# Kernel tuning notes

Measured on AMD Instinct MI355X. Metric: run time of the kernel, lower is better.

Reference implementation:

```python
import jax, jax.numpy as jnp
import numpy as np

B, S, D, H, HD, K, FF, G, E = 2, 2048, 512, 8, 64, 31, 2048, 4, 2
EPS = 1e-6


def _layer_norm(x, scale, bias):
    m = jnp.mean(x, axis=-1, keepdims=True)
    v = jnp.var(x, axis=-1, keepdims=True)
    return (x - m) * jax.lax.rsqrt(v + EPS) * scale + bias


def _forward(x, group_ids, p):
    (ln1_s, ln1_b, ck, cb, ln2_s, ln2_b,
     wq, bq, wk, bk, wv, bv, wo, bo, w1, b1, w2, b2) = p
    # ---- conv sublayer: LN -> Conv1d(SAME) -> gelu -> residual ----
    r = x
    h = _layer_norm(x, ln1_s, ln1_b)
    h = jax.lax.conv_general_dilated(h, ck, (1,), 'SAME',
                                     dimension_numbers=('NWC', 'WIO', 'NWC')) + cb
    x = jax.nn.gelu(h) + r
    # ---- self-attention sublayer: LN -> MHA -> residual ----
    r = x
    h = _layer_norm(x, ln2_s, ln2_b)
    q = jnp.einsum('bsd,dhk->bshk', h, wq) + bq   # [B,S,H,HD]
    k = jnp.einsum('bsd,dhk->bshk', h, wk) + bk
    v = jnp.einsum('bsd,dhk->bshk', h, wv) + bv
    scale = jnp.asarray(1.0 / np.sqrt(HD), h.dtype)
    att = jax.nn.softmax(jnp.einsum('bqhk,bshk->bhqs', q, k) * scale, axis=-1)
    o = jnp.einsum('bhqs,bshk->bqhk', att, v)
    x = jnp.einsum('bqhk,hkd->bqd', o, wo) + bo + r
    # ---- MoE sublayer: group tokens -> per-group experts -> mean -> combine ----
    r = x
    xf = x.reshape(-1, D)            # [N, D]
    gid = group_ids.reshape(-1)      # [N]
    # Each token routed by group_id gets the mean over that group's E experts.
    hid = jax.nn.gelu(jnp.einsum('nd,gedf->genf', xf, w1) + b1[:, :, None, :])  # [G,E,N,FF]
    ye = jnp.einsum('genf,gefd->gend', hid, w2) + b2[:, :, None, :]             # [G,E,N,D]
    yg = ye.mean(axis=1)                                                        # [G,N,D]
    sel = yg[gid, jnp.arange(gid.shape[0])]                                     # [N,D] combine by group id
    return sel.reshape(B, S, D) + r


def setup_inputs() -> dict:
    key = jax.random.key(0)
    ks = jax.random.split(key, 12)
    std = 0.02
    f32 = jnp.float32
    return {
        'x': jax.random.normal(ks[0], (B, S, D), f32),
        'group_ids': jax.random.randint(ks[1], (B, S), 0, G, jnp.int32),
        'ln1_scale': jnp.ones((D,), f32), 'ln1_bias': jnp.zeros((D,), f32),
        'conv_kernel': jax.random.normal(ks[2], (K, D, D), f32) * std,
        'conv_bias': jnp.zeros((D,), f32),
        'ln2_scale': jnp.ones((D,), f32), 'ln2_bias': jnp.zeros((D,), f32),
        'wq': jax.random.normal(ks[3], (D, H, HD), f32) * std, 'bq': jnp.zeros((H, HD), f32),
        'wk': jax.random.normal(ks[4], (D, H, HD), f32) * std, 'bk': jnp.zeros((H, HD), f32),
        'wv': jax.random.normal(ks[5], (D, H, HD), f32) * std, 'bv': jnp.zeros((H, HD), f32),
        'wo': jax.random.normal(ks[6], (H, HD, D), f32) * std, 'bo': jnp.zeros((D,), f32),
        'w1': jax.random.normal(ks[7], (G, E, D, FF), f32) * std, 'b1': jnp.zeros((G, E, FF), f32),
        'w2': jax.random.normal(ks[8], (G, E, FF, D), f32) * std, 'b2': jnp.zeros((G, E, D), f32),
    }


def reference(x, group_ids, ln1_scale, ln1_bias, conv_kernel, conv_bias,
              ln2_scale, ln2_bias, wq, bq, wk, bk, wv, bv, wo, bo,
              w1, b1, w2, b2):
    p = (ln1_scale, ln1_bias, conv_kernel, conv_bias, ln2_scale, ln2_bias,
         wq, bq, wk, bk, wv, bv, wo, bo, w1, b1, w2, b2)
    return _forward(x, group_ids, p)
```

## Files before the change

kernel.cpp:

```cpp
#include <hip/hip_runtime.h>
#include <hip/hip_bf16.h>
#include <math.h>
#include <stdint.h>

namespace {

constexpr int B_ = 2, S_ = 2048, D_ = 512, H_ = 8, HD_ = 64, K_ = 31,
              FF_ = 2048, G_ = 4, E_ = 2;
constexpr int N_ = B_ * S_;
constexpr int SP_ = S_ + 30;
constexpr float EPS_ = 1e-6f;
constexpr int PADCAP_ = 4608;

typedef __bf16 bf16x8 __attribute__((ext_vector_type(8)));
typedef unsigned short u16x8 __attribute__((ext_vector_type(8)));
typedef unsigned short u16x4 __attribute__((ext_vector_type(4)));
typedef float f32x4 __attribute__((ext_vector_type(4)));

__device__ __forceinline__ uint16_t f2bf(float f) {
  union { float f; uint32_t u; } v; v.f = f;
  uint32_t r = v.u + 0x7FFFu + ((v.u >> 16) & 1u);
  return (uint16_t)(r >> 16);
}
__device__ __forceinline__ float bf2f(uint16_t u) {
  union { uint32_t u; float f; } v; v.u = (uint32_t)u << 16;
  return v.f;
}

__device__ __forceinline__ float gelu_f(float x) {
  const float c = 0.7978845608028654f;
  return 0.5f * x * (1.0f + tanhf(c * (x + 0.044715f * x * x * x)));
}

#define GLOAD_LDS16(gsrc, ldst)                                              \
  __builtin_amdgcn_global_load_lds(                                          \
      (const __attribute__((address_space(1))) void*)(gsrc),                 \
      (__attribute__((address_space(3))) void*)(ldst), 16, 0, 0)

#define VMCNT(n) asm volatile("s_waitcnt vmcnt(" #n ")" ::: "memory")
#define MEMBAR asm volatile("" ::: "memory")
#define BARRIER __builtin_amdgcn_s_barrier()

__device__ __forceinline__ void kstep_swz(const char* As, const char* Bs,
                                          int wr, int wc, int l15, int g,
                                          f32x4 acc[4][4]) {
#pragma unroll
  for (int ks = 0; ks < 2; ++ks) {
    int co = (((ks << 2) | g) ^ (l15 & 7)) << 4;
    bf16x8 a[4], b[4];
#pragma unroll
    for (int m = 0; m < 4; ++m)
      a[m] = *(const bf16x8*)(As + (wr * 64 + m * 16 + l15) * 128 + co);
#pragma unroll
    for (int n = 0; n < 4; ++n)
      b[n] = *(const bf16x8*)(Bs + (wc * 64 + n * 16 + l15) * 128 + co);
#pragma unroll
    for (int m = 0; m < 4; ++m)
#pragma unroll
      for (int n = 0; n < 4; ++n)
        acc[m][n] = __builtin_amdgcn_mfma_f32_16x16x32_bf16(a[m], b[n], acc[m][n], 0, 0, 0);
  }
}

template <int NK>
__device__ __forceinline__ void gemm_k_dbuf64(const uint16_t* Ab, int lda,
                                              const uint16_t* Bb, int ldb,
                                              int t, int wr, int wc, int l15, int g,
                                              uint16_t (*As)[8192], uint16_t (*Bs)[8192],
                                              f32x4 acc[4][4]) {
  int r8 = t >> 3, clog = (t & 7) ^ (r8 & 7);
  int ubase = (t & ~63) * 8;
  auto stage = [&](int k0, int buf) {
#pragma unroll
    for (int pi = 0; pi < 4; ++pi) {
      int row = pi * 32 + r8;
      GLOAD_LDS16(Ab + (size_t)row * lda + k0 + clog * 8, As[buf] + pi * 2048 + ubase);
      GLOAD_LDS16(Bb + (size_t)row * ldb + k0 + clog * 8, Bs[buf] + pi * 2048 + ubase);
    }
  };
  stage(0, 0);
  int cur = 0;
  for (int ki = 0; ki < NK; ++ki) {
    if (ki + 1 < NK) {
      stage((ki + 1) * 64, cur ^ 1);
      VMCNT(8);
    } else {
      VMCNT(0);
    }
    BARRIER; MEMBAR;
    kstep_swz((const char*)As[cur], (const char*)Bs[cur], wr, wc, l15, g, acc);
    MEMBAR; BARRIER;
    cur ^= 1;
  }
}

__global__ __launch_bounds__(256) void prep_kernel(
    const float* __restrict__ ck, const float* __restrict__ wq,
    const float* __restrict__ wk, const float* __restrict__ wv,
    const float* __restrict__ wo, const float* __restrict__ w1,
    const float* __restrict__ w2, uint16_t* __restrict__ ckT,
    uint16_t* __restrict__ wqkvT, uint16_t* __restrict__ woT,
    uint16_t* __restrict__ w1T, uint16_t* __restrict__ w2T,
    uint16_t* __restrict__ Hpad, uint16_t* __restrict__ x2bf) {
  int bi = blockIdx.x, t = threadIdx.x;
  if (bi >= 25344) {
    int j4 = bi - 25344;
    uint16_t* dst;
    if (j4 < 60) {
      int b = j4 / 30, j = j4 % 30;
      int row = b * SP_ + (j < 15 ? j : 2048 + j);
      dst = Hpad + (size_t)row * D_;
    } else {
      dst = x2bf + (size_t)N_ * D_;
    }
    dst[t] = 0;
    dst[t + 256] = 0;
    return;
  }
  const float* src;
  uint16_t* dst;
  int R, C, r0, c0;
  if (bi < 7936) {
    int z = bi >> 8, tile = bi & 255;
    R = 512; C = 512;
    c0 = (tile & 15) * 32; r0 = (tile >> 4) * 32;
    src = ck + (size_t)z * 262144; dst = ckT + (size_t)z * 262144;
  } else if (bi < 8960) {
    int idx = bi - 7936, mat = idx >> 8, tile = idx & 255;
    R = 512; C = 512;
    c0 = (tile & 15) * 32; r0 = (tile >> 4) * 32;
    src = mat == 0 ? wq : (mat == 1 ? wk : (mat == 2 ? wv : wo));
    dst = mat == 3 ? woT : wqkvT + (size_t)mat * 262144;
  } else if (bi < 17152) {
    int idx = bi - 8960, z = idx >> 10, tile = idx & 1023;
    R = 512; C = 2048;
    c0 = (tile & 63) * 32; r0 = (tile >> 6) * 32;
    src = w1 + (size_t)z * 1048576; dst = w1T + (size_t)z * 1048576;
  } else {
    int idx = bi - 17152, z = idx >> 10, tile = idx & 1023;
    R = 2048; C = 512;
    c0 = (tile & 15) * 32; r0 = (tile >> 4) * 32;
    src = w2 + (size_t)z * 1048576; dst = w2T + (size_t)z * 1048576;
  }
  __shared__ float tile[32][33];
  int tc = t & 31, tr = t >> 5;
#pragma unroll
  for (int i = 0; i < 4; ++i) {
    int r = tr + i * 8;
    tile[r][tc] = src[(size_t)(r0 + r) * C + c0 + tc];
  }
  __syncthreads();
#pragma unroll
  for (int i = 0; i < 4; ++i) {
    int rr = tr + i * 8;
    dst[(size_t)(c0 + rr) * R + r0 + tc] = f2bf(tile[tc][rr]);
  }
}

__global__ __launch_bounds__(256) void ln_bf16_kernel(
    const float* __restrict__ in, uint16_t* __restrict__ out,
    const float* __restrict__ scale, const float* __restrict__ bias, int hpad) {
  int row = blockIdx.x;
  const float* xr = in + (size_t)row * D_;
  int t = threadIdx.x;
  float v0 = xr[t], v1 = xr[t + 256];
  float s = v0 + v1, sq = v0 * v0 + v1 * v1;
  for (int o = 32; o > 0; o >>= 1) {
    s += __shfl_down(s, o);
    sq += __shfl_down(sq, o);
  }
  __shared__ float sm[8];
  __shared__ float mr[2];
  int lane = t & 63, wid = t >> 6;
  if (lane == 0) { sm[wid] = s; sm[wid + 4] = sq; }
  __syncthreads();
  if (t == 0) {
    float ts = sm[0] + sm[1] + sm[2] + sm[3];
    float tq = sm[4] + sm[5] + sm[6] + sm[7];
    float m = ts / D_;
    mr[0] = m;
    mr[1] = rsqrtf(tq / D_ - m * m + EPS_);
  }
  __syncthreads();
  float m = mr[0], rs = mr[1];
  size_t drow = hpad ? ((size_t)(row >> 11) * SP_ + 15 + (row & 2047)) : (size_t)row;
  uint16_t* orow = out + drow * D_;
  orow[t] = f2bf((v0 - m) * rs * scale[t] + bias[t]);
  orow[t + 256] = f2bf((v1 - m) * rs * scale[t + 256] + bias[t + 256]);
}

__global__ __launch_bounds__(512) void conv_mfma_kernel(
    const uint16_t* __restrict__ Hpad, const uint16_t* __restrict__ ckT,
    uint16_t* __restrict__ Pout) {
  __shared__ __align__(16) uint16_t As[2][20480];
  __shared__ __align__(16) uint16_t Bs[2][16384];
  int bid = blockIdx.x;
  int ks = bid & 7, tmn = bid >> 3, tm = tmn & 15, tn = tmn >> 4;
  int t = threadIdx.x;
  int w = t >> 6, l = t & 63, l15 = l & 15, g = l >> 4;
  int wr = w >> 2, wc = w & 3;
  int row0 = tm * 256, b = row0 >> 11, s0 = row0 & 2047;
  int kb = ks * 4, ntap = (ks == 7) ? 3 : 4;
  const uint16_t* Abase = Hpad + (size_t)(b * SP_ + s0 + kb) * D_;
  int r8 = t >> 3, clog = (t & 7) ^ (r8 & 7);
  int ubase = (t & ~63) * 8;
  f32x4 acc[8][4] = {};

  auto stageA = [&](int d0, int buf) {
#pragma unroll
    for (int pi = 0; pi < 5; ++pi)
      GLOAD_LDS16(Abase + (size_t)(pi * 64 + r8) * D_ + d0 + clog * 8,
                  As[buf] + pi * 4096 + ubase);
  };
  auto stageB = [&](int k, int d0, int buf) {
    const uint16_t* Bk = ckT + (size_t)k * D_ * D_ + (size_t)(tn * 256) * D_;
#pragma unroll
    for (int pi = 0; pi < 4; ++pi)
      GLOAD_LDS16(Bk + (size_t)(pi * 64 + r8) * D_ + d0 + clog * 8,
                  Bs[buf] + pi * 4096 + ubase);
  };

  stageA(0, 0);
  stageB(kb, 0, 0);
  int acur = 0, bcur = 0;
  for (int di = 0; di < 8; ++di) {
    int d0 = di * 64;
    for (int i = 0; i < ntap; ++i) {
      if (i + 1 < ntap) {
        stageB(kb + i + 1, d0, bcur ^ 1);
        VMCNT(4);
      } else if (di + 1 < 8) {
        stageA(d0 + 64, acur ^ 1);
        stageB(kb, d0 + 64, bcur ^ 1);
        VMCNT(9);
      } else {
        VMCNT(0);
      }
      BARRIER; MEMBAR;
      const char* Ac = (const char*)As[acur];
      const char* Bc = (const char*)Bs[bcur];
#pragma unroll
      for (int kk = 0; kk < 2; ++kk) {
        int cA = (((kk << 2) | g) ^ ((i + l15) & 7)) << 4;
        int cB = (((kk << 2) | g) ^ (l15 & 7)) << 4;
        bf16x8 a[8], bb[4];
#pragma unroll
        for (int m = 0; m < 8; ++m)
          a[m] = *(const bf16x8*)(Ac + (i + wr * 128 + m * 16 + l15) * 128 + cA);
#pragma unroll
        for (int n = 0; n < 4; ++n)
          bb[n] = *(const bf16x8*)(Bc + (wc * 64 + n * 16 + l15) * 128 + cB);
#pragma unroll
        for (int m = 0; m < 8; ++m)
#pragma unroll
          for (int n = 0; n < 4; ++n)
            acc[m][n] = __builtin_amdgcn_mfma_f32_16x16x32_bf16(a[m], bb[n], acc[m][n], 0, 0, 0);
      }
      MEMBAR; BARRIER;
      bcur ^= 1;
    }
    acur ^= 1;
  }
  uint16_t* P = Pout + (size_t)ks * N_ * D_;
#pragma unroll
  for (int m = 0; m < 8; ++m) {
    int r = row0 + wr * 128 + m * 16 + g * 4;
#pragma unroll
    for (int n = 0; n < 4; ++n) {
      int c = tn * 256 + wc * 64 + n * 16 + l15;
#pragma unroll
      for (int j = 0; j < 4; ++j)
        P[(size_t)(r + j) * D_ + c] = f2bf(acc[m][n][j]);
    }
  }
}

__global__ __launch_bounds__(256) void conv_epi_kernel(
    const uint16_t* __restrict__ P, const float* __restrict__ cb,
    const float* __restrict__ xres, float* __restrict__ x1) {
  int idx = blockIdx.x * 256 + threadIdx.x;
  float vsum[8] = {};
#pragma unroll
  for (int q = 0; q < 8; ++q) {
    u16x8 pv = ((const u16x8*)(P + (size_t)q * N_ * D_))[idx];
#pragma unroll
    for (int j = 0; j < 8; ++j) vsum[j] += bf2f(pv[j]);
  }
  int base = idx * 8, dbase = base & (D_ - 1);
  const float* bias = cb + dbase;
  const float* xr = xres + base;
  float* o = x1 + base;
#pragma unroll
  for (int j = 0; j < 8; ++j)
    o[j] = gelu_f(vsum[j] + bias[j]) + xr[j];
}

__global__ __launch_bounds__(256) void gemm_qkv_kernel(
    const uint16_t* __restrict__ A, const uint16_t* __restrict__ BT,
    const float* __restrict__ bq, const float* __restrict__ bk,
    const float* __restrict__ bv, uint16_t* __restrict__ Qb,
    uint16_t* __restrict__ Kb, uint16_t* __restrict__ VT) {
  __shared__ __align__(16) uint16_t As[2][8192], Bs[2][8192];
  int tm = blockIdx.x, tn = blockIdx.y;
  int t = threadIdx.x;
  int w = t >> 6, l = t & 63, l15 = l & 15, g = l >> 4;
  int wr = w >> 1, wc = w & 1;
  int row0 = tm * 128;
  f32x4 acc[4][4] = {};
  gemm_k_dbuf64<8>(A + (size_t)row0 * D_, D_, BT + (size_t)(tn * 128) * D_, D_,
                   t, wr, wc, l15, g, As, Bs, acc);
  int sel = tn >> 2, col0 = (tn & 3) * 128;
  if (sel < 2) {
    uint16_t* dst = sel == 0 ? Qb : Kb;
    const float* bias = sel == 0 ? bq : bk;
    float scl = sel == 0 ? 0.125f : 1.0f;
#pragma unroll
    for (int m = 0; m < 4; ++m) {
      int r = row0 + wr * 64 + m * 16 + g * 4;
#pragma unroll
      for (int n = 0; n < 4; ++n) {
        int c = col0 + wc * 64 + n * 16 + l15;
#pragma unroll
        for (int j = 0; j < 4; ++j)
          dst[(size_t)(r + j) * D_ + c] = f2bf((acc[m][n][j] + bias[c]) * scl);
      }
    }
  } else {
#pragma unroll
    for (int m = 0; m < 4; ++m) {
      int tb = row0 + wr * 64 + m * 16 + g * 4;
      int b = tb >> 11, s = tb & 2047;
#pragma unroll
      for (int n = 0; n < 4; ++n) {
        int c = col0 + wc * 64 + n * 16 + l15;
        int hh = c >> 6, d = c & 63;
        u16x4 pack;
#pragma unroll
        for (int j = 0; j < 4; ++j) pack[j] = f2bf(acc[m][n][j] + bv[c]);
        *(u16x4*)(VT + ((size_t)((b * H_ + hh) * HD_ + d) * S_ + s)) = pack;
      }
    }
  }
}

__global__ __launch_bounds__(256) void gemm_wo_kernel(
    const uint16_t* __restrict__ A, const uint16_t* __restrict__ BT,
    const float* __restrict__ bo, const float* __restrict__ res,
    float* __restrict__ out, uint16_t* __restrict__ x2bf) {
  __shared__ __align__(16) uint16_t As[2][8192], Bs[2][8192];
  int tm = blockIdx.x, tn = blockIdx.y;
  int t = threadIdx.x;
  int w = t >> 6, l = t & 63, l15 = l & 15, g = l >> 4;
  int wr = w >> 1, wc = w & 1;
  int row0 = tm * 128;
  f32x4 acc[4][4] = {};
  gemm_k_dbuf64<8>(A + (size_t)row0 * D_, D_, BT + (size_t)(tn * 128) * D_, D_,
                   t, wr, wc, l15, g, As, Bs, acc);
#pragma unroll
  for (int m = 0; m < 4; ++m) {
    int r = row0 + wr * 64 + m * 16 + g * 4;
#pragma unroll
    for (int n = 0; n < 4; ++n) {
      int c = tn * 128 + wc * 64 + n * 16 + l15;
#pragma unroll
      for (int j = 0; j < 4; ++j) {
        float v = acc[m][n][j] + bo[c] + res[(size_t)(r + j) * D_ + c];
        out[(size_t)(r + j) * D_ + c] = v;
        x2bf[(size_t)(r + j) * D_ + c] = f2bf(v);
      }
    }
  }
}

__global__ __launch_bounds__(256) void attn_mfma_kernel(
    const uint16_t* __restrict__ Qbf, const uint16_t* __restrict__ Kbf,
    const uint16_t* __restrict__ VT, uint16_t* __restrict__ obf) {
  __shared__ __align__(16) uint16_t Ks[2][4096];
  __shared__ __align__(16) uint16_t Vt[2][4096];
  __shared__ __align__(16) uint16_t Plds[4096];
  int qt = blockIdx.x, h = blockIdx.y, b = blockIdx.z;
  int t = threadIdx.x, w = t >> 6, l = t & 63;
  int l15 = l & 15, g = l >> 4;
  int qbase = b * S_ + qt * 64;
  bf16x8 qb_[2];
  {
    const uint16_t* qp = Qbf + (size_t)(qbase + w * 16 + l15) * D_ + h * HD_;
#pragma unroll
    for (int ks = 0; ks < 2; ++ks)
      qb_[ks] = *(const bf16x8*)(qp + ks * 32 + g * 8);
  }
  const uint16_t* Kbase = Kbf + (size_t)(b * S_) * D_ + h * HD_;
  const uint16_t* Vbase = VT + (size_t)((b * H_ + h) * HD_) * S_;
  int r0 = t >> 3, slot = t & 7, r1 = r0 + 32;
  int sb0 = (slot * 16) ^ ((r0 & 7) << 4);
  int sb1 = (slot * 16) ^ ((r1 & 7) << 4);
  int ldst = (t & ~63) * 16;

  auto stage_kv = [&](int kt, int buf) {
    const uint16_t* Kp = Kbase + (size_t)(kt * 64) * D_;
    const uint16_t* Vp = Vbase + kt * 64;
    GLOAD_LDS16((const char*)(Kp + (size_t)r0 * D_) + sb0, (char*)Ks[buf] + ldst);
    GLOAD_LDS16((const char*)(Kp + (size_t)r1 * D_) + sb1, (char*)Ks[buf] + 4096 + ldst);
    GLOAD_LDS16((const char*)(Vp + (size_t)r0 * S_) + sb0, (char*)Vt[buf] + ldst);
    GLOAD_LDS16((const char*)(Vp + (size_t)r1 * S_) + sb1, (char*)Vt[buf] + 4096 + ldst);
  };

  f32x4 acc_o[4] = {};
  float m_run = -INFINITY, l_run = 0.f;
  char* Pw = (char*)Plds + w * 2048;

  stage_kv(0, 0);
  int cur = 0;
  for (int kt = 0; kt < S_ / 64; ++kt) {
    if (kt + 1 < S_ / 64) {
      stage_kv(kt + 1, cur ^ 1);
      VMCNT(4);
    } else {
      VMCNT(0);
    }
    BARRIER; MEMBAR;
    const char* KsC = (const char*)Ks[cur];
    const char* VtC = (const char*)Vt[cur];
    f32x4 accs[4] = {};
#pragma unroll
    for (int ks = 0; ks < 2; ++ks) {
#pragma unroll
      for (int m = 0; m < 4; ++m) {
        int row = m * 16 + l15;
        bf16x8 kf = *(const bf16x8*)(KsC +
                        (row * 128 + ((ks * 64 + g * 16) ^ ((row & 7) << 4))));
        accs[m] = __builtin_amdgcn_mfma_f32_16x16x32_bf16(kf, qb_[ks], accs[m], 0, 0, 0);
      }
    }
    float mx = accs[0][0];
#pragma unroll
    for (int m = 0; m < 4; ++m)
#pragma unroll
      for (int j = 0; j < 4; ++j) mx = fmaxf(mx, accs[m][j]);
    mx = fmaxf(mx, __shfl_xor(mx, 16));
    mx = fmaxf(mx, __shfl_xor(mx, 32));
    float mnew = fmaxf(m_run, mx);
    float corr = __expf(m_run - mnew);
    m_run = mnew;
    float sum = 0.f;
#pragma unroll
    for (int m = 0; m < 4; ++m) {
      float p0 = __expf(accs[m][0] - mnew);
      float p1 = __expf(accs[m][1] - mnew);
      float p2 = __expf(accs[m][2] - mnew);
      float p3 = __expf(accs[m][3] - mnew);
      sum += (p0 + p1) + (p2 + p3);
      uint2 pk;
      pk.x = (uint32_t)f2bf(p0) | ((uint32_t)f2bf(p1) << 16);
      pk.y = (uint32_t)f2bf(p2) | ((uint32_t)f2bf(p3) << 16);
      *(uint2*)(Pw + (l15 * 128 + ((m * 32 + g * 8) ^ ((l15 & 7) << 4)))) = pk;
    }
    sum += __shfl_xor(sum, 16);
    sum += __shfl_xor(sum, 32);
    l_run = l_run * corr + sum;
    float cj[4];
#pragma unroll
    for (int j = 0; j < 4; ++j) cj[j] = __shfl(corr, g * 4 + j);
#pragma unroll
    for (int n = 0; n < 4; ++n)
#pragma unroll
      for (int j = 0; j < 4; ++j) acc_o[n][j] *= cj[j];
#pragma unroll
    for (int ks = 0; ks < 2; ++ks) {
      bf16x8 pa = *(const bf16x8*)(Pw +
                      (l15 * 128 + ((ks * 64 + g * 16) ^ ((l15 & 7) << 4))));
#pragma unroll
      for (int n = 0; n < 4; ++n) {
        int d = n * 16 + l15;
        bf16x8 vb = *(const bf16x8*)(VtC +
                        (d * 128 + ((ks * 64 + g * 16) ^ ((d & 7) << 4))));
        acc_o[n] = __builtin_amdgcn_mfma_f32_16x16x32_bf16(pa, vb, acc_o[n], 0, 0, 0);
      }
    }
    MEMBAR; BARRIER;
    cur ^= 1;
  }
#pragma unroll
  for (int j = 0; j < 4; ++j) {
    float lr = __shfl(l_run, g * 4 + j);
    float inv = 1.f / lr;
    uint16_t* op = obf + (size_t)(qbase + w * 16 + g * 4 + j) * D_ + h * HD_;
#pragma unroll
    for (int n = 0; n < 4; ++n)
      op[n * 16 + l15] = f2bf(acc_o[n][j] * inv);
  }
}

__global__ __launch_bounds__(1024) void bucket_kernel(
    const int* __restrict__ gid, int* __restrict__ list, int* __restrict__ poff) {
  __shared__ int cnt[G_], cur[G_];
  int t = threadIdx.x;
  if (t < G_) cnt[t] = 0;
  __syncthreads();
  for (int i = t; i < N_; i += 1024) atomicAdd(&cnt[gid[i]], 1);
  __syncthreads();
  if (t == 0) {
    int off = 0;
    for (int g = 0; g < G_; ++g) {
      poff[g] = off;
      cur[g] = off;
      off += (cnt[g] + 127) & ~127;
    }
    poff[G_] = off;
  }
  __syncthreads();
  for (int i = t; i < PADCAP_; i += 1024) list[i] = N_;
  __syncthreads();
  for (int i = t; i < N_; i += 1024) {
    int p = atomicAdd(&cur[gid[i]], 1);
    list[p] = i;
  }
}

__global__ __launch_bounds__(256) void ff1_mfma_kernel(
    const uint16_t* __restrict__ X, const uint16_t* __restrict__ w1T,
    const float* __restrict__ b1, const int* __restrict__ list,
    const int* __restrict__ poff, uint16_t* __restrict__ hid) {
  __shared__ __align__(16) uint16_t As[2][8192], Bs[2][8192];
  int tm = blockIdx.x, tn = blockIdx.y, e = blockIdx.z;
  int slot0 = tm * 128;
  if (slot0 >= poff[G_]) return;
  int g_ = 0;
#pragma unroll
  for (int gg = 1; gg < G_; ++gg) g_ += (slot0 >= poff[gg]);
  int t = threadIdx.x;
  int w = t >> 6, l = t & 63, l15 = l & 15, g = l >> 4;
  int wr = w >> 1, wc = w & 1;
  int r8 = t >> 3, clog = (t & 7) ^ (r8 & 7);
  int ubase = (t & ~63) * 8;
  int tok[4];
#pragma unroll
  for (int pi = 0; pi < 4; ++pi) tok[pi] = list[slot0 + pi * 32 + r8];
  const uint16_t* Bb = w1T + ((size_t)(g_ * E_ + e) * FF_ + tn * 128) * D_;
  f32x4 acc[4][4] = {};
  auto stage = [&](int k0, int buf) {
#pragma unroll
    for (int pi = 0; pi < 4; ++pi) {
      GLOAD_LDS16(X + (size_t)tok[pi] * D_ + k0 + clog * 8, As[buf] + pi * 2048 + ubase);
      GLOAD_LDS16(Bb + (size_t)(pi * 32 + r8) * D_ + k0 + clog * 8,
                  Bs[buf] + pi * 2048 + ubase);
    }
  };
  stage(0, 0);
  int cur = 0;
  for (int ki = 0; ki < 8; ++ki) {
    if (ki + 1 < 8) {
      stage((ki + 1) * 64, cur ^ 1);
      VMCNT(8);
    } else {
      VMCNT(0);
    }
    BARRIER; MEMBAR;
    kstep_swz((const char*)As[cur], (const char*)Bs[cur], wr, wc, l15, g, acc);
    MEMBAR; BARRIER;
    cur ^= 1;
  }
  const float* bias = b1 + (size_t)(g_ * E_ + e) * FF_;
  uint16_t* hidE = hid + (size_t)e * PADCAP_ * FF_;
#pragma unroll
  for (int m = 0; m < 4; ++m) {
    int r = slot0 + wr * 64 + m * 16 + g * 4;
#pragma unroll
    for (int n = 0; n < 4; ++n) {
      int c = tn * 128 + wc * 64 + n * 16 + l15;
#pragma unroll
      for (int j = 0; j < 4; ++j)
        hidE[(size_t)(r + j) * FF_ + c] = f2bf(gelu_f(acc[m][n][j] + bias[c]));
    }
  }
}

__global__ __launch_bounds__(256) void ff2_mfma_kernel(
    const uint16_t* __restrict__ hid, const uint16_t* __restrict__ w2T,
    const float* __restrict__ b2, const int* __restrict__ list,
    const int* __restrict__ poff, float* __restrict__ out) {
  __shared__ __align__(16) uint16_t As[2][8192], Bs[2][8192];
  int tm = blockIdx.x, tn = blockIdx.y, e = blockIdx.z;
  int slot0 = tm * 128;
  if (slot0 >= poff[G_]) return;
  int g_ = 0;
#pragma unroll
  for (int gg = 1; gg < G_; ++gg) g_ += (slot0 >= poff[gg]);
  int t = threadIdx.x;
  int w = t >> 6, l = t & 63, l15 = l & 15, g = l >> 4;
  int wr = w >> 1, wc = w & 1;
  f32x4 acc[4][4] = {};
  const uint16_t* Ab = hid + ((size_t)e * PADCAP_ + slot0) * FF_;
  const uint16_t* Bb = w2T + (size_t)(g_ * E_ + e) * D_ * FF_ + (size_t)(tn * 128) * FF_;
  gemm_k_dbuf64<32>(Ab, FF_, Bb, FF_, t, wr, wc, l15, g, As, Bs, acc);
  const float* be = b2 + (size_t)(g_ * E_ + e) * D_;
#pragma unroll
  for (int m = 0; m < 4; ++m) {
    int rbase = slot0 + wr * 64 + m * 16 + g * 4;
#pragma unroll
    for (int j = 0; j < 4; ++j) {
      int tok = list[rbase + j];
      if (tok >= N_) continue;
#pragma unroll
      for (int n = 0; n < 4; ++n) {
        int c = tn * 128 + wc * 64 + n * 16 + l15;
        atomicAdd(&out[(size_t)tok * D_ + c], 0.5f * (acc[m][n][j] + be[c]));
      }
    }
  }
}

}

extern "C" void kernel_launch(void* const* d_in, const int* in_sizes, int n_in,
                              void* d_out, int out_size, void* d_ws, size_t ws_size,
                              hipStream_t stream) {
  const float* x = (const float*)d_in[0];
  const int* gid = (const int*)d_in[1];
  const float* ln1s = (const float*)d_in[2];
  const float* ln1b = (const float*)d_in[3];
  const float* ck = (const float*)d_in[4];
  const float* cb = (const float*)d_in[5];
  const float* ln2s = (const float*)d_in[6];
  const float* ln2b = (const float*)d_in[7];
  const float* wq = (const float*)d_in[8];
  const float* bq = (const float*)d_in[9];
  const float* wk = (const float*)d_in[10];
  const float* bk = (const float*)d_in[11];
  const float* wv = (const float*)d_in[12];
  const float* bv = (const float*)d_in[13];
  const float* wo = (const float*)d_in[14];
  const float* bo = (const float*)d_in[15];
  const float* w1 = (const float*)d_in[16];
  const float* b1 = (const float*)d_in[17];
  const float* w2 = (const float*)d_in[18];
  const float* b2 = (const float*)d_in[19];
  float* out = (float*)d_out;

  char* ws = (char*)d_ws;
  char* A = ws;
  uint16_t* P = (uint16_t*)A;
  uint16_t* ln2bf = (uint16_t*)A;
  uint16_t* Qbf = (uint16_t*)(A + (4ull << 20));
  uint16_t* Kbf = (uint16_t*)(A + (8ull << 20));
  uint16_t* VT = (uint16_t*)(A + (12ull << 20));
  uint16_t* obf = (uint16_t*)(A + (16ull << 20));
  uint16_t* hidbf = (uint16_t*)A;

  float* x1 = (float*)(ws + (38ull << 20));
  uint16_t* Hpad = (uint16_t*)(ws + (46ull << 20));
  uint16_t* ckT = (uint16_t*)(ws + (51ull << 20));
  uint16_t* wqkvT = (uint16_t*)(ws + (67ull << 20));
  uint16_t* woT = (uint16_t*)(ws + (69ull << 20));
  uint16_t* w1T = (uint16_t*)(ws + (70ull << 20));
  uint16_t* w2T = (uint16_t*)(ws + (86ull << 20));
  uint16_t* x2bf = (uint16_t*)(ws + (102ull << 20));
  int* list = (int*)(ws + (107ull << 20));
  int* poff = list + PADCAP_;

  prep_kernel<<<25405, 256, 0, stream>>>(ck, wq, wk, wv, wo, w1, w2,
                                         ckT, wqkvT, woT, w1T, w2T, Hpad, x2bf);
  bucket_kernel<<<1, 1024, 0, stream>>>(gid, list, poff);

  ln_bf16_kernel<<<N_, 256, 0, stream>>>(x, Hpad, ln1s, ln1b, 1);
  conv_mfma_kernel<<<256, 512, 0, stream>>>(Hpad, ckT, P);
  conv_epi_kernel<<<1024, 256, 0, stream>>>(P, cb, x, x1);

  ln_bf16_kernel<<<N_, 256, 0, stream>>>(x1, ln2bf, ln2s, ln2b, 0);
  gemm_qkv_kernel<<<dim3(32, 12), 256, 0, stream>>>(ln2bf, wqkvT, bq, bk, bv, Qbf, Kbf, VT);
  attn_mfma_kernel<<<dim3(S_ / 64, H_, B_), 256, 0, stream>>>(Qbf, Kbf, VT, obf);
  gemm_wo_kernel<<<dim3(32, 4), 256, 0, stream>>>(obf, woT, bo, x1, out, x2bf);

  ff1_mfma_kernel<<<dim3(36, 16, 2), 256, 0, stream>>>(x2bf, w1T, b1, list, poff, hidbf);
  ff2_mfma_kernel<<<dim3(36, 4, 2), 256, 0, stream>>>(hidbf, w2T, b2, list, poff, out);
}
```

Before: 313.9 us.

## Fuse LN and bucketing into prep, fuse conv epilogue with LN2, retile attention and FF2

Folds the first layer norm and the group bucketing into the weight-prep launch, and merges the conv epilogue with the second layer norm so each row is normalized in registers with wave shuffles. Attention goes to 128-query tiles with 512 threads, and FF2 splits K in half to double its grid. MFMA blocks are also wrapped in s_setprio to favour matrix issue. The aim is fewer launches and intermediate round-trips plus better occupancy, at the cost of more atomics in FF2 and a bucketing step now run by 256 threads instead of 1024.

```diff
diff --git a/kernel.cpp b/kernel.cpp
--- a/kernel.cpp
+++ b/kernel.cpp
@@ -40,6 +40,8 @@
 #define VMCNT(n) asm volatile("s_waitcnt vmcnt(" #n ")" ::: "memory")
 #define MEMBAR asm volatile("" ::: "memory")
 #define BARRIER __builtin_amdgcn_s_barrier()
+#define PRIO1 __builtin_amdgcn_s_setprio(1)
+#define PRIO0 __builtin_amdgcn_s_setprio(0)
 
 __device__ __forceinline__ void kstep_swz(const char* As, const char* Bs,
                                           int wr, int wc, int l15, int g,
@@ -54,11 +56,13 @@
 #pragma unroll
     for (int n = 0; n < 4; ++n)
       b[n] = *(const bf16x8*)(Bs + (wc * 64 + n * 16 + l15) * 128 + co);
+    PRIO1;
 #pragma unroll
     for (int m = 0; m < 4; ++m)
 #pragma unroll
       for (int n = 0; n < 4; ++n)
         acc[m][n] = __builtin_amdgcn_mfma_f32_16x16x32_bf16(a[m], b[n], acc[m][n], 0, 0, 0);
+    PRIO0;
   }
 }
 
@@ -101,8 +105,64 @@
     const float* __restrict__ w2, uint16_t* __restrict__ ckT,
     uint16_t* __restrict__ wqkvT, uint16_t* __restrict__ woT,
     uint16_t* __restrict__ w1T, uint16_t* __restrict__ w2T,
-    uint16_t* __restrict__ Hpad, uint16_t* __restrict__ x2bf) {
+    uint16_t* __restrict__ Hpad, uint16_t* __restrict__ x2bf,
+    const float* __restrict__ x, const float* __restrict__ ln1s,
+    const float* __restrict__ ln1b, const int* __restrict__ gid,
+    int* __restrict__ list, int* __restrict__ poff) {
   int bi = blockIdx.x, t = threadIdx.x;
+  if (bi >= 25406) {
+    int row = bi - 25406;
+    const float* xr = x + (size_t)row * D_;
+    float v0 = xr[t], v1 = xr[t + 256];
+    float s = v0 + v1, sq = v0 * v0 + v1 * v1;
+    for (int o = 32; o > 0; o >>= 1) {
+      s += __shfl_down(s, o);
+      sq += __shfl_down(sq, o);
+    }
+    __shared__ float sm[8];
+    __shared__ float mr[2];
+    int lane = t & 63, wid = t >> 6;
+    if (lane == 0) { sm[wid] = s; sm[wid + 4] = sq; }
+    __syncthreads();
+    if (t == 0) {
+      float ts = sm[0] + sm[1] + sm[2] + sm[3];
+      float tq = sm[4] + sm[5] + sm[6] + sm[7];
+      float m = ts / D_;
+      mr[0] = m;
+      mr[1] = rsqrtf(tq / D_ - m * m + EPS_);
+    }
+    __syncthreads();
+    float m = mr[0], rs = mr[1];
+    size_t drow = (size_t)(row >> 11) * SP_ + 15 + (row & 2047);
+    uint16_t* orow = Hpad + drow * D_;
+    orow[t] = f2bf((v0 - m) * rs * ln1s[t] + ln1b[t]);
+    orow[t + 256] = f2bf((v1 - m) * rs * ln1s[t + 256] + ln1b[t + 256]);
+    return;
+  }
+  if (bi == 25405) {
+    __shared__ int cnt[G_], cur[G_];
+    if (t < G_) cnt[t] = 0;
+    __syncthreads();
+    for (int i = t; i < N_; i += 256) atomicAdd(&cnt[gid[i]], 1);
+    __syncthreads();
+    if (t == 0) {
+      int off = 0;
+      for (int g = 0; g < G_; ++g) {
+        poff[g] = off;
+        cur[g] = off;
+        off += (cnt[g] + 127) & ~127;
+      }
+      poff[G_] = off;
+    }
+    __syncthreads();
+    for (int i = t; i < PADCAP_; i += 256) list[i] = N_;
+    __syncthreads();
+    for (int i = t; i < N_; i += 256) {
+      int p = atomicAdd(&cur[gid[i]], 1);
+      list[p] = i;
+    }
+    return;
+  }
   if (bi >= 25344) {
     int j4 = bi - 25344;
     uint16_t* dst;
@@ -157,38 +217,6 @@
   }
 }
 
-__global__ __launch_bounds__(256) void ln_bf16_kernel(
-    const float* __restrict__ in, uint16_t* __restrict__ out,
-    const float* __restrict__ scale, const float* __restrict__ bias, int hpad) {
-  int row = blockIdx.x;
-  const float* xr = in + (size_t)row * D_;
-  int t = threadIdx.x;
-  float v0 = xr[t], v1 = xr[t + 256];
-  float s = v0 + v1, sq = v0 * v0 + v1 * v1;
-  for (int o = 32; o > 0; o >>= 1) {
-    s += __shfl_down(s, o);
-    sq += __shfl_down(sq, o);
-  }
-  __shared__ float sm[8];
-  __shared__ float mr[2];
-  int lane = t & 63, wid = t >> 6;
-  if (lane == 0) { sm[wid] = s; sm[wid + 4] = sq; }
-  __syncthreads();
-  if (t == 0) {
-    float ts = sm[0] + sm[1] + sm[2] + sm[3];
-    float tq = sm[4] + sm[5] + sm[6] + sm[7];
-    float m = ts / D_;
-    mr[0] = m;
-    mr[1] = rsqrtf(tq / D_ - m * m + EPS_);
-  }
-  __syncthreads();
-  float m = mr[0], rs = mr[1];
-  size_t drow = hpad ? ((size_t)(row >> 11) * SP_ + 15 + (row & 2047)) : (size_t)row;
-  uint16_t* orow = out + drow * D_;
-  orow[t] = f2bf((v0 - m) * rs * scale[t] + bias[t]);
-  orow[t + 256] = f2bf((v1 - m) * rs * scale[t + 256] + bias[t + 256]);
-}
-
 __global__ __launch_bounds__(512) void conv_mfma_kernel(
     const uint16_t* __restrict__ Hpad, const uint16_t* __restrict__ ckT,
     uint16_t* __restrict__ Pout) {
@@ -250,11 +278,13 @@
 #pragma unroll
         for (int n = 0; n < 4; ++n)
           bb[n] = *(const bf16x8*)(Bc + (wc * 64 + n * 16 + l15) * 128 + cB);
+        PRIO1;
 #pragma unroll
         for (int m = 0; m < 8; ++m)
 #pragma unroll
           for (int n = 0; n < 4; ++n)
             acc[m][n] = __builtin_amdgcn_mfma_f32_16x16x32_bf16(a[m], bb[n], acc[m][n], 0, 0, 0);
+        PRIO0;
       }
       MEMBAR; BARRIER;
       bcur ^= 1;
@@ -275,24 +305,46 @@
   }
 }
 
-__global__ __launch_bounds__(256) void conv_epi_kernel(
+__global__ __launch_bounds__(256) void epi_ln_kernel(
     const uint16_t* __restrict__ P, const float* __restrict__ cb,
-    const float* __restrict__ xres, float* __restrict__ x1) {
-  int idx = blockIdx.x * 256 + threadIdx.x;
-  float vsum[8] = {};
+    const float* __restrict__ xres, const float* __restrict__ ln2s,
+    const float* __restrict__ ln2b, float* __restrict__ x1,
+    uint16_t* __restrict__ ln2bf) {
+  int t = threadIdx.x;
+  int row = blockIdx.x * 4 + (t >> 6);
+  int l = t & 63, d0 = l * 8;
+  size_t base = (size_t)row * D_ + d0;
+  float v[8] = {};
 #pragma unroll
   for (int q = 0; q < 8; ++q) {
-    u16x8 pv = ((const u16x8*)(P + (size_t)q * N_ * D_))[idx];
-#pragma unroll
-    for (int j = 0; j < 8; ++j) vsum[j] += bf2f(pv[j]);
-  }
-  int base = idx * 8, dbase = base & (D_ - 1);
-  const float* bias = cb + dbase;
-  const float* xr = xres + base;
-  float* o = x1 + base;
+    u16x8 pv = *(const u16x8*)(P + (size_t)q * N_ * D_ + base);
+#pragma unroll
+    for (int j = 0; j < 8; ++j) v[j] += bf2f(pv[j]);
+  }
+  float s = 0.f, sq = 0.f;
+#pragma unroll
+  for (int j = 0; j < 8; ++j) {
+    float xv = xres[base + j];
+    float vv = gelu_f(v[j] + cb[d0 + j]) + xv;
+    v[j] = vv;
+    s += vv;
+    sq += vv * vv;
+  }
+  float4 o0 = {v[0], v[1], v[2], v[3]};
+  float4 o1 = {v[4], v[5], v[6], v[7]};
+  *(float4*)(x1 + base) = o0;
+  *(float4*)(x1 + base + 4) = o1;
+  for (int o = 1; o < 64; o <<= 1) {
+    s += __shfl_xor(s, o);
+    sq += __shfl_xor(sq, o);
+  }
+  float m = s / D_;
+  float rs = rsqrtf(sq / D_ - m * m + EPS_);
+  u16x8 ob;
 #pragma unroll
   for (int j = 0; j < 8; ++j)
-    o[j] = gelu_f(vsum[j] + bias[j]) + xr[j];
+    ob[j] = f2bf((v[j] - m) * rs * ln2s[d0 + j] + ln2b[d0 + j]);
+  *(u16x8*)(ln2bf + base) = ob;
 }
 
 __global__ __launch_bounds__(256) void gemm_qkv_kernel(
@@ -372,16 +424,16 @@
   }
 }
 
-__global__ __launch_bounds__(256) void attn_mfma_kernel(
+__global__ __launch_bounds__(512) void attn_mfma_kernel(
     const uint16_t* __restrict__ Qbf, const uint16_t* __restrict__ Kbf,
     const uint16_t* __restrict__ VT, uint16_t* __restrict__ obf) {
   __shared__ __align__(16) uint16_t Ks[2][4096];
   __shared__ __align__(16) uint16_t Vt[2][4096];
-  __shared__ __align__(16) uint16_t Plds[4096];
+  __shared__ __align__(16) uint16_t Plds[8192];
   int qt = blockIdx.x, h = blockIdx.y, b = blockIdx.z;
   int t = threadIdx.x, w = t >> 6, l = t & 63;
   int l15 = l & 15, g = l >> 4;
-  int qbase = b * S_ + qt * 64;
+  int qbase = b * S_ + qt * 128;
   bf16x8 qb_[2];
   {
     const uint16_t* qp = Qbf + (size_t)(qbase + w * 16 + l15) * D_ + h * HD_;
@@ -391,18 +443,15 @@
   }
   const uint16_t* Kbase = Kbf + (size_t)(b * S_) * D_ + h * HD_;
   const uint16_t* Vbase = VT + (size_t)((b * H_ + h) * HD_) * S_;
-  int r0 = t >> 3, slot = t & 7, r1 = r0 + 32;
+  int r0 = t >> 3, slot = t & 7;
   int sb0 = (slot * 16) ^ ((r0 & 7) << 4);
-  int sb1 = (slot * 16) ^ ((r1 & 7) << 4);
   int ldst = (t & ~63) * 16;
 
   auto stage_kv = [&](int kt, int buf) {
     const uint16_t* Kp = Kbase + (size_t)(kt * 64) * D_;
     const uint16_t* Vp = Vbase + kt * 64;
     GLOAD_LDS16((const char*)(Kp + (size_t)r0 * D_) + sb0, (char*)Ks[buf] + ldst);
-    GLOAD_LDS16((const char*)(Kp + (size_t)r1 * D_) + sb1, (char*)Ks[buf] + 4096 + ldst);
     GLOAD_LDS16((const char*)(Vp + (size_t)r0 * S_) + sb0, (char*)Vt[buf] + ldst);
-    GLOAD_LDS16((const char*)(Vp + (size_t)r1 * S_) + sb1, (char*)Vt[buf] + 4096 + ldst);
   };
 
   f32x4 acc_o[4] = {};
@@ -414,7 +463,7 @@
   for (int kt = 0; kt < S_ / 64; ++kt) {
     if (kt + 1 < S_ / 64) {
       stage_kv(kt + 1, cur ^ 1);
-      VMCNT(4);
+      VMCNT(2);
     } else {
       VMCNT(0);
     }
@@ -429,7 +478,9 @@
         int row = m * 16 + l15;
         bf16x8 kf = *(const bf16x8*)(KsC +
                         (row * 128 + ((ks * 64 + g * 16) ^ ((row & 7) << 4))));
+        PRIO1;
         accs[m] = __builtin_amdgcn_mfma_f32_16x16x32_bf16(kf, qb_[ks], accs[m], 0, 0, 0);
+        PRIO0;
       }
     }
     float mx = accs[0][0];
@@ -474,7 +525,9 @@
         int d = n * 16 + l15;
         bf16x8 vb = *(const bf16x8*)(VtC +
                         (d * 128 + ((ks * 64 + g * 16) ^ ((d & 7) << 4))));
+        PRIO1;
         acc_o[n] = __builtin_amdgcn_mfma_f32_16x16x32_bf16(pa, vb, acc_o[n], 0, 0, 0);
+        PRIO0;
       }
     }
     MEMBAR; BARRIER;
@@ -488,32 +541,6 @@
 #pragma unroll
     for (int n = 0; n < 4; ++n)
       op[n * 16 + l15] = f2bf(acc_o[n][j] * inv);
-  }
-}
-
-__global__ __launch_bounds__(1024) void bucket_kernel(
-    const int* __restrict__ gid, int* __restrict__ list, int* __restrict__ poff) {
-  __shared__ int cnt[G_], cur[G_];
-  int t = threadIdx.x;
-  if (t < G_) cnt[t] = 0;
-  __syncthreads();
-  for (int i = t; i < N_; i += 1024) atomicAdd(&cnt[gid[i]], 1);
-  __syncthreads();
-  if (t == 0) {
-    int off = 0;
-    for (int g = 0; g < G_; ++g) {
-      poff[g] = off;
-      cur[g] = off;
-      off += (cnt[g] + 127) & ~127;
-    }
-    poff[G_] = off;
-  }
-  __syncthreads();
-  for (int i = t; i < PADCAP_; i += 1024) list[i] = N_;
-  __syncthreads();
-  for (int i = t; i < N_; i += 1024) {
-    int p = atomicAdd(&cur[gid[i]], 1);
-    list[p] = i;
   }
 }
 
@@ -580,7 +607,8 @@
     const float* __restrict__ b2, const int* __restrict__ list,
     const int* __restrict__ poff, float* __restrict__ out) {
   __shared__ __align__(16) uint16_t As[2][8192], Bs[2][8192];
-  int tm = blockIdx.x, tn = blockIdx.y, e = blockIdx.z;
+  int tm = blockIdx.x, tn = blockIdx.y, z = blockIdx.z;
+  int e = z >> 1, kh = z & 1;
   int slot0 = tm * 128;
   if (slot0 >= poff[G_]) return;
   int g_ = 0;
@@ -590,10 +618,12 @@
   int w = t >> 6, l = t & 63, l15 = l & 15, g = l >> 4;
   int wr = w >> 1, wc = w & 1;
   f32x4 acc[4][4] = {};
-  const uint16_t* Ab = hid + ((size_t)e * PADCAP_ + slot0) * FF_;
-  const uint16_t* Bb = w2T + (size_t)(g_ * E_ + e) * D_ * FF_ + (size_t)(tn * 128) * FF_;
-  gemm_k_dbuf64<32>(Ab, FF_, Bb, FF_, t, wr, wc, l15, g, As, Bs, acc);
+  const uint16_t* Ab = hid + ((size_t)e * PADCAP_ + slot0) * FF_ + kh * 1024;
+  const uint16_t* Bb = w2T + (size_t)(g_ * E_ + e) * D_ * FF_ +
+                       (size_t)(tn * 128) * FF_ + kh * 1024;
+  gemm_k_dbuf64<16>(Ab, FF_, Bb, FF_, t, wr, wc, l15, g, As, Bs, acc);
   const float* be = b2 + (size_t)(g_ * E_ + e) * D_;
+  float bs = (kh == 0) ? 0.5f : 0.f;
 #pragma unroll
   for (int m = 0; m < 4; ++m) {
     int rbase = slot0 + wr * 64 + m * 16 + g * 4;
@@ -604,7 +634,7 @@
 #pragma unroll
       for (int n = 0; n < 4; ++n) {
         int c = tn * 128 + wc * 64 + n * 16 + l15;
-        atomicAdd(&out[(size_t)tok * D_ + c], 0.5f * (acc[m][n][j] + be[c]));
+        atomicAdd(&out[(size_t)tok * D_ + c], 0.5f * acc[m][n][j] + bs * be[c]);
       }
     }
   }
@@ -640,11 +670,11 @@
   char* ws = (char*)d_ws;
   char* A = ws;
   uint16_t* P = (uint16_t*)A;
-  uint16_t* ln2bf = (uint16_t*)A;
-  uint16_t* Qbf = (uint16_t*)(A + (4ull << 20));
-  uint16_t* Kbf = (uint16_t*)(A + (8ull << 20));
-  uint16_t* VT = (uint16_t*)(A + (12ull << 20));
-  uint16_t* obf = (uint16_t*)(A + (16ull << 20));
+  uint16_t* ln2bf = (uint16_t*)(A + (32ull << 20));
+  uint16_t* Qbf = (uint16_t*)A;
+  uint16_t* Kbf = (uint16_t*)(A + (4ull << 20));
+  uint16_t* VT = (uint16_t*)(A + (8ull << 20));
+  uint16_t* obf = (uint16_t*)(A + (12ull << 20));
   uint16_t* hidbf = (uint16_t*)A;
 
   float* x1 = (float*)(ws + (38ull << 20));
@@ -658,19 +688,17 @@
   int* list = (int*)(ws + (107ull << 20));
   int* poff = list + PADCAP_;
 
-  prep_kernel<<<25405, 256, 0, stream>>>(ck, wq, wk, wv, wo, w1, w2,
-                                         ckT, wqkvT, woT, w1T, w2T, Hpad, x2bf);
-  bucket_kernel<<<1, 1024, 0, stream>>>(gid, list, poff);
-
-  ln_bf16_kernel<<<N_, 256, 0, stream>>>(x, Hpad, ln1s, ln1b, 1);
+  prep_kernel<<<29502, 256, 0, stream>>>(ck, wq, wk, wv, wo, w1, w2,
+                                         ckT, wqkvT, woT, w1T, w2T, Hpad, x2bf,
+                                         x, ln1s, ln1b, gid, list, poff);
+
   conv_mfma_kernel<<<256, 512, 0, stream>>>(Hpad, ckT, P);
-  conv_epi_kernel<<<1024, 256, 0, stream>>>(P, cb, x, x1);
-
-  ln_bf16_kernel<<<N_, 256, 0, stream>>>(x1, ln2bf, ln2s, ln2b, 0);
+  epi_ln_kernel<<<1024, 256, 0, stream>>>(P, cb, x, ln2s, ln2b, x1, ln2bf);
+
   gemm_qkv_kernel<<<dim3(32, 12), 256, 0, stream>>>(ln2bf, wqkvT, bq, bk, bv, Qbf, Kbf, VT);
-  attn_mfma_kernel<<<dim3(S_ / 64, H_, B_), 256, 0, stream>>>(Qbf, Kbf, VT, obf);
+  attn_mfma_kernel<<<dim3(S_ / 128, H_, B_), 512, 0, stream>>>(Qbf, Kbf, VT, obf);
   gemm_wo_kernel<<<dim3(32, 4), 256, 0, stream>>>(obf, woT, bo, x1, out, x2bf);
 
   ff1_mfma_kernel<<<dim3(36, 16, 2), 256, 0, stream>>>(x2bf, w1T, b1, list, poff, hidbf);
-  ff2_mfma_kernel<<<dim3(36, 4, 2), 256, 0, stream>>>(hidbf, w2T, b2, list, poff, out);
-}
+  ff2_mfma_kernel<<<dim3(36, 4, 4), 256, 0, stream>>>(hidbf, w2T, b2, list, poff, out);
+}
```

New measurement: 341.8 us. 1.09x slower.
